# Kernel optimization log

Measured on AMD Instinct MI355X. Metric: run time of the kernel, lower is better.

Reference implementation:

```python
import jax, jax.numpy as jnp
import numpy as np

B, A, NOBS, H1, HX, NACT = 16384, 32, 2, 128, 64, 5
NEIGHBORHOOD = 2.0
GRID_X, GRID_Y = 3, 7


def setup_inputs() -> dict:
    key = jax.random.key(0)
    ks = jax.random.split(key, 6)
    s = 0.1
    return {
        "obs": jax.random.uniform(ks[0], (B, A, NOBS), dtype=jnp.float32),
        # per-agent weights, stored [A, in, out] (torch Linear weight is [out,in])
        "W1": jax.random.normal(ks[1], (A, NOBS, H1), dtype=jnp.float32) * s,
        "b1": jnp.zeros((A, H1), dtype=jnp.float32),
        "W2": jax.random.normal(ks[2], (A, H1, HX), dtype=jnp.float32) * s,
        "b2": jnp.zeros((A, HX), dtype=jnp.float32),
        "Wc": jax.random.normal(ks[3], (A, 2 * HX, HX), dtype=jnp.float32) * s,
        "bc": jnp.zeros((A, HX), dtype=jnp.float32),
        "Wd": jax.random.normal(ks[4], (A, HX, NACT), dtype=jnp.float32) * s,
        "bd": jnp.zeros((A, NACT), dtype=jnp.float32),
    }


def reference(obs, W1, b1, W2, b2, Wc, bc, Wd, bd):
    # --- neighbor mask from L1 distance on rescaled positions ---
    scales = jnp.array([GRID_X - 1.0, GRID_Y - 1.0], dtype=obs.dtype)
    pos = obs * scales  # [B, A, 2]
    dists = jnp.sum(jnp.abs(pos[:, :, None, :] - pos[:, None, :, :]), axis=-1)  # [B, A, A]
    mask = ((dists > 0.0) & (dists < NEIGHBORHOOD)).astype(obs.dtype)  # [B, A, A]

    # --- per-agent encoder MLP: Linear(2,128)+ReLU, Linear(128,64)+ReLU ---
    h = jax.nn.relu(jnp.einsum('bai,aio->bao', obs, W1) + b1)   # [B, A, 128]
    hidden = jax.nn.relu(jnp.einsum('bai,aio->bao', h, W2) + b2)  # [B, A, 64]

    # --- k=1 communication round: masked neighbor mean, then per-agent Linear+Tanh ---
    total = jnp.einsum('baj,bjh->bah', mask, hidden)  # [B, A, 64]
    J = jnp.sum(mask, axis=-1)                         # [B, A]
    J = jnp.where(J > 0.0, J, 1.0)
    comms = total / J[..., None]
    comm_input = jnp.concatenate([hidden, comms], axis=-1)  # [B, A, 128]
    hidden = jnp.tanh(jnp.einsum('bai,aio->bao', comm_input, Wc) + bc)  # [B, A, 64]

    # --- per-agent decoder Linear(64, n_actions) ---
    q = jnp.einsum('bah,aho->bao', hidden, Wd) + bd  # [B, A, NACT]
    return q
```

## Files before the change

### kernel.cpp

```cpp
#include <hip/hip_runtime.h>

#define NAGENTS 32
#define NOBSV   2
#define H1D     128
#define HXD     64
#define NACTD   5

typedef _Float16 h8 __attribute__((ext_vector_type(8)));
typedef float f32x4 __attribute__((ext_vector_type(4)));


__global__ __launch_bounds__(256, 4) void k0_prep(
    const float* __restrict__ W2, const float* __restrict__ Wc,
    h8* __restrict__ wfrag)
{
    const int a = blockIdx.x;
    const int tid = threadIdx.x;
    #pragma unroll
    for (int mat = 0; mat < 2; ++mat) {
        const float* src = (mat == 0 ? W2 : Wc) + (size_t)a * (H1D * HXD);
        h8* dhi = wfrag + ((size_t)(mat * NAGENTS + a) * 2 + 0) * 1024;
        h8* dlo = wfrag + ((size_t)(mat * NAGENTS + a) * 2 + 1) * 1024;
        #pragma unroll
        for (int s4 = 0; s4 < 4; ++s4) {
            const int s  = tid + s4 * 256;
            const int fi = s >> 6, ln = s & 63;
            const int k0  = (fi >> 2) * 32 + (ln >> 4) * 8;
            const int col = (fi & 3) * 16 + (ln & 15);
            h8 whi, wlo;
            #pragma unroll
            for (int j = 0; j < 8; ++j) {
                float w = src[(size_t)(k0 + j) * HXD + col];
                _Float16 hi = (_Float16)w;
                whi[j] = hi;
                wlo[j] = (_Float16)(w - (float)hi);
            }
            dhi[s] = whi;
            dlo[s] = wlo;
        }
    }
}

__global__ __launch_bounds__(256, 4) void k1_encoder(
    const float* __restrict__ obs, const float* __restrict__ W1,
    const float* __restrict__ b1, const float* __restrict__ W2,
    const float* __restrict__ b2, _Float16* __restrict__ ci,
    const h8* __restrict__ wfrag)
{
    __shared__ h8    s_wf[2][16][64];
    __shared__ float s_w1a[H1D], s_w1b[H1D], s_b1[H1D], s_b2[HXD];
    __shared__ float s_ob[128][2];

    const int a   = blockIdx.x;
    const int r0  = blockIdx.y * 128;
    const int tid = threadIdx.x;
    const int wv  = tid >> 6, lane = tid & 63;
    const int l15 = lane & 15, lq = lane >> 4;

    {
        const float* w1p = W1 + a * (NOBSV * H1D);
        if (tid < H1D) {
            s_w1a[tid] = w1p[tid];
            s_w1b[tid] = w1p[H1D + tid];
            s_b1[tid]  = b1[a * H1D + tid];
        } else if (tid < H1D + HXD) {
            s_b2[tid - H1D] = b2[a * HXD + (tid - H1D)];
        }
        if (tid < 128) {
            const float2 ov = *reinterpret_cast<const float2*>(
                obs + ((size_t)(r0 + tid) * NAGENTS + a) * NOBSV);
            s_ob[tid][0] = ov.x; s_ob[tid][1] = ov.y;
        }
        if (wfrag) {
            const h8* srcf = wfrag + (size_t)a * 2048;
            h8* dstf = &s_wf[0][0][0];
            #pragma unroll
            for (int c = 0; c < 8; ++c) dstf[tid + c * 256] = srcf[tid + c * 256];
        } else {
            const float* wsrc = W2 + (size_t)a * (H1D * HXD);
            #pragma unroll
            for (int s4 = 0; s4 < 4; ++s4) {
                const int s  = tid + s4 * 256;
                const int fi = s >> 6, ln = s & 63;
                const int k0  = (fi >> 2) * 32 + (ln >> 4) * 8;
                const int col = (fi & 3) * 16 + (ln & 15);
                h8 whi, wlo;
                #pragma unroll
                for (int j = 0; j < 8; ++j) {
                    float w = wsrc[(size_t)(k0 + j) * HXD + col];
                    _Float16 hi = (_Float16)w;
                    whi[j] = hi;
                    wlo[j] = (_Float16)(w - (float)hi);
                }
                s_wf[0][fi][ln] = whi;
                s_wf[1][fi][ln] = wlo;
            }
        }
    }
    __syncthreads();

    const float o0r0 = s_ob[wv * 32 + l15][0],      o1r0 = s_ob[wv * 32 + l15][1];
    const float o0r1 = s_ob[wv * 32 + 16 + l15][0], o1r1 = s_ob[wv * 32 + 16 + l15][1];

    f32x4 acc[2][4];
    #pragma unroll
    for (int m = 0; m < 2; ++m)
        #pragma unroll
        for (int n = 0; n < 4; ++n) {
            const float bv = s_b2[n * 16 + l15];
            acc[m][n] = (f32x4){bv, bv, bv, bv};
        }
    #pragma unroll
    for (int kt = 0; kt < 4; ++kt) {
        h8 af0, af1;
        #pragma unroll
        for (int j = 0; j < 8; ++j) {
            const int k = kt * 32 + lq * 8 + j;
            const float wa = s_w1a[k], wb = s_w1b[k], bb = s_b1[k];
            af0[j] = (_Float16)fmaxf(fmaf(o1r0, wb, fmaf(o0r0, wa, bb)), 0.0f);
            af1[j] = (_Float16)fmaxf(fmaf(o1r1, wb, fmaf(o0r1, wa, bb)), 0.0f);
        }
        #pragma unroll
        for (int n = 0; n < 4; ++n) {
            h8 bh = s_wf[0][kt * 4 + n][lane];
            h8 bl = s_wf[1][kt * 4 + n][lane];
            acc[0][n] = __builtin_amdgcn_mfma_f32_16x16x32_f16(af0, bh, acc[0][n], 0, 0, 0);
            acc[1][n] = __builtin_amdgcn_mfma_f32_16x16x32_f16(af1, bh, acc[1][n], 0, 0, 0);
            acc[0][n] = __builtin_amdgcn_mfma_f32_16x16x32_f16(af0, bl, acc[0][n], 0, 0, 0);
            acc[1][n] = __builtin_amdgcn_mfma_f32_16x16x32_f16(af1, bl, acc[1][n], 0, 0, 0);
        }
    }
    #pragma unroll
    for (int m = 0; m < 2; ++m)
        #pragma unroll
        for (int r = 0; r < 4; ++r) {
            const int row = wv * 32 + m * 16 + lq * 4 + r;
            _Float16* dst = ci + ((size_t)(r0 + row) * NAGENTS + a) * 128;
            #pragma unroll
            for (int n = 0; n < 4; ++n)
                dst[n * 16 + l15] = (_Float16)fmaxf(acc[m][n][r], 0.0f);
        }
}

__global__ __launch_bounds__(256, 2) void k2_comms(
    const float* __restrict__ obs, _Float16* __restrict__ ci)
{
    __shared__ __align__(16) _Float16 s_tt[8][64][40];
    __shared__ __align__(16) _Float16 s_m[8][32][40];
    __shared__ float s_o[8][66];
    __shared__ float s_J[8][32];

    const int r0  = blockIdx.x * 8;
    const int tid = threadIdx.x;
    const int wv  = tid >> 6, lane = tid & 63;
    const int l15 = lane & 15, lq = lane >> 4;

    if (tid < 128) {
        const float4 v = reinterpret_cast<const float4*>(obs + (size_t)r0 * NAGENTS * NOBSV)[tid];
        const int row = tid >> 4, seg = tid & 15;
        *reinterpret_cast<float4*>(&s_o[row][seg * 4]) = v;
    }
    __syncthreads();

    const int row = tid >> 5;
    const int u   = tid & 31;

    {
        const h8* src = reinterpret_cast<const h8*>(
            ci + ((size_t)(r0 + row) * NAGENTS + u) * 128);
        #pragma unroll
        for (int c = 0; c < 8; ++c) {
            h8 v = src[c];
            #pragma unroll
            for (int e = 0; e < 8; ++e) s_tt[row][c * 8 + e][u] = v[e];
        }
    }
    {
        unsigned int bits = 0u;
        const double xi = (double)s_o[row][u * 2 + 0] * 2.0;
        const double yi = (double)s_o[row][u * 2 + 1] * 6.0;
        #pragma unroll
        for (int j = 0; j < NAGENTS; ++j) {
            double xj = (double)s_o[row][j * 2 + 0] * 2.0;
            double yj = (double)s_o[row][j * 2 + 1] * 6.0;
            double d = fabs(xi - xj) + fabs(yi - yj);
            if (d > 0.0 && d < 2.0) bits |= (1u << j);
        }
        s_J[row][u] = fmaxf((float)__popc(bits), 1.0f);
        #pragma unroll
        for (int c = 0; c < 4; ++c) {
            h8 mv;
            #pragma unroll
            for (int e = 0; e < 8; ++e)
                mv[e] = ((bits >> (c * 8 + e)) & 1u) ? (_Float16)1.0f : (_Float16)0.0f;
            *reinterpret_cast<h8*>(&s_m[row][u][c * 8]) = mv;
        }
    }
    asm volatile("s_waitcnt lgkmcnt(0)" ::: "memory");
    __builtin_amdgcn_sched_barrier(0);

    #pragma unroll
    for (int rr = 0; rr < 2; ++rr) {
        const int rw = wv * 2 + rr;
        h8 a0 = *reinterpret_cast<const h8*>(&s_m[rw][l15][lq * 8]);
        h8 a1 = *reinterpret_cast<const h8*>(&s_m[rw][16 + l15][lq * 8]);
        f32x4 acc[2][4];
        #pragma unroll
        for (int m = 0; m < 2; ++m)
            #pragma unroll
            for (int n = 0; n < 4; ++n) acc[m][n] = (f32x4){0.f, 0.f, 0.f, 0.f};
        #pragma unroll
        for (int n = 0; n < 4; ++n) {
            h8 b = *reinterpret_cast<const h8*>(&s_tt[rw][n * 16 + l15][lq * 8]);
            acc[0][n] = __builtin_amdgcn_mfma_f32_16x16x32_f16(a0, b, acc[0][n], 0, 0, 0);
            acc[1][n] = __builtin_amdgcn_mfma_f32_16x16x32_f16(a1, b, acc[1][n], 0, 0, 0);
        }
        #pragma unroll
        for (int m = 0; m < 2; ++m)
            #pragma unroll
            for (int r = 0; r < 4; ++r) {
                const int ai = m * 16 + lq * 4 + r;
                const float Jv = s_J[rw][ai];
                _Float16* dst = ci + ((size_t)(r0 + rw) * NAGENTS + ai) * 128 + 64;
                #pragma unroll
                for (int n = 0; n < 4; ++n)
                    dst[n * 16 + l15] = (_Float16)(acc[m][n][r] / Jv);
            }
    }
}

__global__ __launch_bounds__(256, 4) void k3_head(
    const _Float16* __restrict__ ci,
    const float* __restrict__ Wc, const float* __restrict__ bc,
    const float* __restrict__ Wd, const float* __restrict__ bd,
    float* __restrict__ out, const h8* __restrict__ wfrag)
{
    __shared__ h8    s_wf[2][16][64];
    __shared__ float s_wd[HXD][8];
    __shared__ float s_bc[HXD];
    __shared__ float s_bd[8];

    const int a   = blockIdx.x;
    const int r0  = blockIdx.y * 128;
    const int tid = threadIdx.x;
    const int wv  = tid >> 6, lane = tid & 63;
    const int l15 = lane & 15, lq = lane >> 4;

    {
        if (wfrag) {
            const h8* srcf = wfrag + (size_t)(NAGENTS + a) * 2048;
            h8* dstf = &s_wf[0][0][0];
            #pragma unroll
            for (int c = 0; c < 8; ++c) dstf[tid + c * 256] = srcf[tid + c * 256];
        } else {
            const float* wsrc = Wc + (size_t)a * (2 * HXD * HXD);
            #pragma unroll
            for (int s4 = 0; s4 < 4; ++s4) {
                const int s  = tid + s4 * 256;
                const int fi = s >> 6, ln = s & 63;
                const int k0  = (fi >> 2) * 32 + (ln >> 4) * 8;
                const int col = (fi & 3) * 16 + (ln & 15);
                h8 whi, wlo;
                #pragma unroll
                for (int j = 0; j < 8; ++j) {
                    float w = wsrc[(size_t)(k0 + j) * HXD + col];
                    _Float16 hi = (_Float16)w;
                    whi[j] = hi;
                    wlo[j] = (_Float16)(w - (float)hi);
                }
                s_wf[0][fi][ln] = whi;
                s_wf[1][fi][ln] = wlo;
            }
        }
        if (tid < HXD) {
            s_bc[tid] = bc[a * HXD + tid];
            #pragma unroll
            for (int o = 0; o < NACTD; ++o)
                s_wd[tid][o] = Wd[(size_t)a * (HXD * NACTD) + tid * NACTD + o];
        } else if (tid < HXD + NACTD) {
            s_bd[tid - HXD] = bd[a * NACTD + (tid - HXD)];
        }
    }
    __syncthreads();

    const _Float16* rb0 = ci + ((size_t)(r0 + wv * 32 + l15) * NAGENTS + a) * 128;
    const _Float16* rb1 = rb0 + (size_t)16 * NAGENTS * 128;

    f32x4 acc[2][4];
    #pragma unroll
    for (int m = 0; m < 2; ++m)
        #pragma unroll
        for (int n = 0; n < 4; ++n) {
            const float bv = s_bc[n * 16 + l15];
            acc[m][n] = (f32x4){bv, bv, bv, bv};
        }
    #pragma unroll
    for (int kt = 0; kt < 4; ++kt) {
        h8 af0 = *reinterpret_cast<const h8*>(rb0 + kt * 32 + lq * 8);
        h8 af1 = *reinterpret_cast<const h8*>(rb1 + kt * 32 + lq * 8);
        #pragma unroll
        for (int n = 0; n < 4; ++n) {
            h8 bh = s_wf[0][kt * 4 + n][lane];
            h8 bl = s_wf[1][kt * 4 + n][lane];
            acc[0][n] = __builtin_amdgcn_mfma_f32_16x16x32_f16(af0, bh, acc[0][n], 0, 0, 0);
            acc[1][n] = __builtin_amdgcn_mfma_f32_16x16x32_f16(af1, bh, acc[1][n], 0, 0, 0);
            acc[0][n] = __builtin_amdgcn_mfma_f32_16x16x32_f16(af0, bl, acc[0][n], 0, 0, 0);
            acc[1][n] = __builtin_amdgcn_mfma_f32_16x16x32_f16(af1, bl, acc[1][n], 0, 0, 0);
        }
    }

    #pragma unroll
    for (int m = 0; m < 2; ++m)
        #pragma unroll
        for (int r = 0; r < 4; ++r) {
            float qv[NACTD];
            #pragma unroll
            for (int o = 0; o < NACTD; ++o) qv[o] = 0.0f;
            #pragma unroll
            for (int n = 0; n < 4; ++n) {
                const float t = tanhf(acc[m][n][r]);
                const float* wd = s_wd[n * 16 + l15];
                #pragma unroll
                for (int o = 0; o < NACTD; ++o) qv[o] = fmaf(t, wd[o], qv[o]);
            }
            #pragma unroll
            for (int o = 0; o < NACTD; ++o) {
                qv[o] += __shfl_xor(qv[o], 1, 64);
                qv[o] += __shfl_xor(qv[o], 2, 64);
                qv[o] += __shfl_xor(qv[o], 4, 64);
                qv[o] += __shfl_xor(qv[o], 8, 64);
            }
            if (l15 == 0) {
                const int row = wv * 32 + m * 16 + lq * 4 + r;
                float* op = out + ((size_t)(r0 + row) * NAGENTS + a) * NACTD;
                #pragma unroll
                for (int o = 0; o < NACTD; ++o) op[o] = qv[o] + s_bd[o];
            }
        }
}

#define TBATCH  8
#define NWAVES  4
#define BFST    2056
#define HROWST  132
__global__ __launch_bounds__(256, 3) void qnet_fused_fb(
    const float* __restrict__ obs,
    const float* __restrict__ W1, const float* __restrict__ b1,
    const float* __restrict__ W2, const float* __restrict__ b2,
    const float* __restrict__ Wc, const float* __restrict__ bc,
    const float* __restrict__ Wd, const float* __restrict__ bd,
    float* __restrict__ out)
{
    __shared__ float    s_obs[TBATCH][NAGENTS * 2 + 2];
    __shared__ _Float16 s_hid[TBATCH * BFST];
    __shared__ float    s_h[NWAVES][TBATCH][HROWST];

    const int tid  = threadIdx.x;
    const int wave = tid >> 6;
    const int lane = tid & 63;
    const int lb   = lane & 7;
    const int og   = lane >> 3;
    const int b0   = blockIdx.x * TBATCH;

    {
        const float2* src = reinterpret_cast<const float2*>(obs + (size_t)b0 * (NAGENTS * NOBSV));
        float2 v = src[tid];
        s_obs[tid >> 5][(tid & 31) * 2 + 0] = v.x;
        s_obs[tid >> 5][(tid & 31) * 2 + 1] = v.y;
    }
    __syncthreads();

    const int p_a = tid >> 3;
    const int p_b = tid & 7;
    unsigned int bits = 0u;
    float Jf;
    {
        const double xi = (double)s_obs[p_b][p_a * 2 + 0] * 2.0;
        const double yi = (double)s_obs[p_b][p_a * 2 + 1] * 6.0;
        #pragma unroll
        for (int j = 0; j < NAGENTS; ++j) {
            double xj = (double)s_obs[p_b][j * 2 + 0] * 2.0;
            double yj = (double)s_obs[p_b][j * 2 + 1] * 6.0;
            double d = fabs(xi - xj) + fabs(yi - yj);
            if (d > 0.0 && d < 2.0) bits |= (1u << j);
        }
        Jf = fmaxf((float)__popc(bits), 1.0f);
    }

    #pragma unroll 1
    for (int ai = 0; ai < 8; ++ai) {
        const int a = wave * 8 + ai;
        const float o0 = s_obs[lb][a * 2 + 0];
        const float o1 = s_obs[lb][a * 2 + 1];
        {
            const float* __restrict__ w1a = W1 + a * (NOBSV * H1D) + og * 16;
            const float* __restrict__ w1b = w1a + H1D;
            const float* __restrict__ b1p = b1 + a * H1D + og * 16;
            float* hdst = &s_h[wave][lb][og * 16];
            #pragma unroll
            for (int c = 0; c < 4; ++c) {
                float4 wa = *reinterpret_cast<const float4*>(w1a + 4 * c);
                float4 wb = *reinterpret_cast<const float4*>(w1b + 4 * c);
                float4 bv = *reinterpret_cast<const float4*>(b1p + 4 * c);
                float4 hv;
                hv.x = fmaxf(fmaf(o1, wb.x, fmaf(o0, wa.x, bv.x)), 0.0f);
                hv.y = fmaxf(fmaf(o1, wb.y, fmaf(o0, wa.y, bv.y)), 0.0f);
                hv.z = fmaxf(fmaf(o1, wb.z, fmaf(o0, wa.z, bv.z)), 0.0f);
                hv.w = fmaxf(fmaf(o1, wb.w, fmaf(o0, wa.w, bv.w)), 0.0f);
                *reinterpret_cast<float4*>(hdst + 4 * c) = hv;
            }
        }
        asm volatile("s_waitcnt lgkmcnt(0)" ::: "memory");
        __builtin_amdgcn_sched_barrier(0);

        const float* __restrict__ w2p = W2 + a * (H1D * HXD) + og * 8;
        const float* __restrict__ b2p = b2 + a * HXD + og * 8;
        float acc[8];
        {
            float4 bv0 = *reinterpret_cast<const float4*>(b2p + 0);
            float4 bv1 = *reinterpret_cast<const float4*>(b2p + 4);
            acc[0] = bv0.x; acc[1] = bv0.y; acc[2] = bv0.z; acc[3] = bv0.w;
            acc[4] = bv1.x; acc[5] = bv1.y; acc[6] = bv1.z; acc[7] = bv1.w;
        }
        const float* hsrc = &s_h[wave][lb][0];
        #pragma unroll 8
        for (int k = 0; k < H1D; ++k) {
            const float hv = hsrc[k];
            const float* wr = w2p + k * HXD;
            float4 wv0 = *reinterpret_cast<const float4*>(wr + 0);
            float4 wv1 = *reinterpret_cast<const float4*>(wr + 4);
            acc[0] = fmaf(hv, wv0.x, acc[0]);
            acc[1] = fmaf(hv, wv0.y, acc[1]);
            acc[2] = fmaf(hv, wv0.z, acc[2]);
            acc[3] = fmaf(hv, wv0.w, acc[3]);
            acc[4] = fmaf(hv, wv1.x, acc[4]);
            acc[5] = fmaf(hv, wv1.y, acc[5]);
            acc[6] = fmaf(hv, wv1.z, acc[6]);
            acc[7] = fmaf(hv, wv1.w, acc[7]);
        }
        h8 hh;
        #pragma unroll
        for (int i = 0; i < 8; ++i) hh[i] = (_Float16)fmaxf(acc[i], 0.0f);
        *reinterpret_cast<h8*>(&s_hid[lb * BFST + a * HXD + og * 8]) = hh;
    }
    __syncthreads();

    #pragma unroll 1
    for (int ai = 0; ai < 8; ++ai) {
        const int a = wave * 8 + ai;
        const int srcm = ai * 8 + lb;
        const unsigned int mbits = (unsigned int)__shfl((int)bits, srcm, 64);
        const float Jv = __shfl(Jf, srcm, 64);

        float cm8[8];
        #pragma unroll
        for (int i = 0; i < 8; ++i) cm8[i] = 0.0f;
        {
            const _Float16* hrow = &s_hid[lb * BFST + og * 8];
            #pragma unroll 8
            for (int j = 0; j < NAGENTS; ++j) {
                const float m = (float)((mbits >> j) & 1u);
                h8 v = *reinterpret_cast<const h8*>(hrow + j * HXD);
                cm8[0] = fmaf(m, (float)v[0], cm8[0]);
                cm8[1] = fmaf(m, (float)v[1], cm8[1]);
                cm8[2] = fmaf(m, (float)v[2], cm8[2]);
                cm8[3] = fmaf(m, (float)v[3], cm8[3]);
                cm8[4] = fmaf(m, (float)v[4], cm8[4]);
                cm8[5] = fmaf(m, (float)v[5], cm8[5]);
                cm8[6] = fmaf(m, (float)v[6], cm8[6]);
                cm8[7] = fmaf(m, (float)v[7], cm8[7]);
            }
        }
        {
            float* cw = &s_h[wave][lb][og * 8];
            *reinterpret_cast<float4*>(cw + 0) =
                make_float4(cm8[0]/Jv, cm8[1]/Jv, cm8[2]/Jv, cm8[3]/Jv);
            *reinterpret_cast<float4*>(cw + 4) =
                make_float4(cm8[4]/Jv, cm8[5]/Jv, cm8[6]/Jv, cm8[7]/Jv);
        }
        asm volatile("s_waitcnt lgkmcnt(0)" ::: "memory");
        __builtin_amdgcn_sched_barrier(0);

        const float* __restrict__ wcp = Wc + a * (2 * HXD * HXD) + og * 8;
        const float* __restrict__ bcp = bc + a * HXD + og * 8;
        float acc[8];
        {
            float4 bv0 = *reinterpret_cast<const float4*>(bcp + 0);
            float4 bv1 = *reinterpret_cast<const float4*>(bcp + 4);
            acc[0] = bv0.x; acc[1] = bv0.y; acc[2] = bv0.z; acc[3] = bv0.w;
            acc[4] = bv1.x; acc[5] = bv1.y; acc[6] = bv1.z; acc[7] = bv1.w;
        }
        const _Float16* hbase = &s_hid[lb * BFST + a * HXD];
        #pragma unroll 8
        for (int k = 0; k < HXD; ++k) {
            const float ci2 = (float)hbase[k];
            const float* wr = wcp + k * HXD;
            float4 wv0 = *reinterpret_cast<const float4*>(wr + 0);
            float4 wv1 = *reinterpret_cast<const float4*>(wr + 4);
            acc[0] = fmaf(ci2, wv0.x, acc[0]);
            acc[1] = fmaf(ci2, wv0.y, acc[1]);
            acc[2] = fmaf(ci2, wv0.z, acc[2]);
            acc[3] = fmaf(ci2, wv0.w, acc[3]);
            acc[4] = fmaf(ci2, wv1.x, acc[4]);
            acc[5] = fmaf(ci2, wv1.y, acc[5]);
            acc[6] = fmaf(ci2, wv1.z, acc[6]);
            acc[7] = fmaf(ci2, wv1.w, acc[7]);
        }
        #pragma unroll 8
        for (int k2 = 0; k2 < HXD; ++k2) {
            const float ci2 = s_h[wave][lb][k2];
            const float* wr = wcp + (HXD + k2) * HXD;
            float4 wv0 = *reinterpret_cast<const float4*>(wr + 0);
            float4 wv1 = *reinterpret_cast<const float4*>(wr + 4);
            acc[0] = fmaf(ci2, wv0.x, acc[0]);
            acc[1] = fmaf(ci2, wv0.y, acc[1]);
            acc[2] = fmaf(ci2, wv0.z, acc[2]);
            acc[3] = fmaf(ci2, wv0.w, acc[3]);
            acc[4] = fmaf(ci2, wv1.x, acc[4]);
            acc[5] = fmaf(ci2, wv1.y, acc[5]);
            acc[6] = fmaf(ci2, wv1.z, acc[6]);
            acc[7] = fmaf(ci2, wv1.w, acc[7]);
        }
        float qv[NACTD];
        #pragma unroll
        for (int o = 0; o < NACTD; ++o) qv[o] = 0.0f;
        const float* __restrict__ wdp = Wd + a * (HXD * NACTD) + og * 8 * NACTD;
        #pragma unroll
        for (int i = 0; i < 8; ++i) {
            float h2 = tanhf(acc[i]);
            #pragma unroll
            for (int o = 0; o < NACTD; ++o)
                qv[o] = fmaf(h2, wdp[i * NACTD + o], qv[o]);
        }
        #pragma unroll
        for (int o = 0; o < NACTD; ++o) {
            qv[o] += __shfl_xor(qv[o], 8, 64);
            qv[o] += __shfl_xor(qv[o], 16, 64);
            qv[o] += __shfl_xor(qv[o], 32, 64);
        }
        if (og == 0) {
            float* op = out + ((size_t)(b0 + lb) * NAGENTS + a) * NACTD;
            const float* bdp = bd + a * NACTD;
            #pragma unroll
            for (int o = 0; o < NACTD; ++o) op[o] = qv[o] + bdp[o];
        }
    }
}

extern "C" void kernel_launch(void* const* d_in, const int* in_sizes, int n_in,
                              void* d_out, int out_size, void* d_ws, size_t ws_size,
                              hipStream_t stream) {
    (void)out_size;
    if (n_in < 9) return;
    const float* obs = (const float*)d_in[0];
    const float* W1  = (const float*)d_in[1];
    const float* b1v = (const float*)d_in[2];
    const float* W2  = (const float*)d_in[3];
    const float* b2v = (const float*)d_in[4];
    const float* Wc  = (const float*)d_in[5];
    const float* bcv = (const float*)d_in[6];
    const float* Wd  = (const float*)d_in[7];
    const float* bdv = (const float*)d_in[8];
    float* out = (float*)d_out;
    const int Btot = in_sizes[0] / (NAGENTS * NOBSV);

    const size_t ciBytes   = (size_t)Btot * NAGENTS * 128 * 2;
    const size_t fragBytes = (size_t)2 * NAGENTS * 2 * 1024 * 16;
    dim3 blk(256);
    if (ws_size >= ciBytes + fragBytes && (Btot % 128) == 0) {
        _Float16* ci = (_Float16*)d_ws;
        h8* wfrag = (h8*)((char*)d_ws + ciBytes);
        k0_prep<<<dim3(NAGENTS), blk, 0, stream>>>(W2, Wc, wfrag);
        k1_encoder<<<dim3(NAGENTS, Btot / 128), blk, 0, stream>>>(
            obs, W1, b1v, W2, b2v, ci, wfrag);
        k2_comms<<<dim3(Btot / 8), blk, 0, stream>>>(obs, ci);
        k3_head<<<dim3(NAGENTS, Btot / 128), blk, 0, stream>>>(
            ci, Wc, bcv, Wd, bdv, out, wfrag);
    } else if (ws_size >= ciBytes && (Btot % 128) == 0) {
        _Float16* ci = (_Float16*)d_ws;
        k1_encoder<<<dim3(NAGENTS, Btot / 128), blk, 0, stream>>>(
            obs, W1, b1v, W2, b2v, ci, (const h8*)nullptr);
        k2_comms<<<dim3(Btot / 8), blk, 0, stream>>>(obs, ci);
        k3_head<<<dim3(NAGENTS, Btot / 128), blk, 0, stream>>>(
            ci, Wc, bcv, Wd, bdv, out, (const h8*)nullptr);
    } else {
        qnet_fused_fb<<<dim3(Btot / TBATCH), dim3(256), 0, stream>>>(
            obs, W1, b1v, W2, b2v, Wc, bcv, Wd, bdv, out);
    }
}
```

Before: 117.5 us.

## Read prepped weight fragments from global memory directly and use fast tanh

The encoder and head kernels no longer stage the 32KB hi/lo fp16 weight fragments in shared memory. Each wave now loads its MFMA B operands straight from the workspace through the cache, and launch bounds rise from 4 to 6 blocks per CU to use the freed LDS for occupancy. The head kernel replaces tanhf with an exp2/rcp approximation, and the comms kernel stores a reciprocal neighbor count so it multiplies instead of divides. The no-prep fallback path is removed. The risks are redundant global/L2 traffic, since every wave re-reads the same fragments, and slightly lower tanh accuracy.

```diff
diff --git a/kernel.cpp b/kernel.cpp
--- a/kernel.cpp
+++ b/kernel.cpp
@@ -9,6 +9,11 @@
 typedef _Float16 h8 __attribute__((ext_vector_type(8)));
 typedef float f32x4 __attribute__((ext_vector_type(4)));
 
+
+static __device__ __forceinline__ float fast_tanh(float x) {
+    float e = __builtin_amdgcn_exp2f(x * 2.885390081777927f);
+    return fmaf(-2.0f, __builtin_amdgcn_rcpf(e + 1.0f), 1.0f);
+}
 
 __global__ __launch_bounds__(256, 4) void k0_prep(
     const float* __restrict__ W2, const float* __restrict__ Wc,
@@ -41,13 +46,11 @@
     }
 }
 
-__global__ __launch_bounds__(256, 4) void k1_encoder(
+__global__ __launch_bounds__(256, 6) void k1_encoder(
     const float* __restrict__ obs, const float* __restrict__ W1,
-    const float* __restrict__ b1, const float* __restrict__ W2,
-    const float* __restrict__ b2, _Float16* __restrict__ ci,
-    const h8* __restrict__ wfrag)
+    const float* __restrict__ b1, const float* __restrict__ b2,
+    _Float16* __restrict__ ci, const h8* __restrict__ wfrag)
 {
-    __shared__ h8    s_wf[2][16][64];
     __shared__ float s_w1a[H1D], s_w1b[H1D], s_b1[H1D], s_b2[HXD];
     __shared__ float s_ob[128][2];
 
@@ -71,33 +74,10 @@
                 obs + ((size_t)(r0 + tid) * NAGENTS + a) * NOBSV);
             s_ob[tid][0] = ov.x; s_ob[tid][1] = ov.y;
         }
-        if (wfrag) {
-            const h8* srcf = wfrag + (size_t)a * 2048;
-            h8* dstf = &s_wf[0][0][0];
-            #pragma unroll
-            for (int c = 0; c < 8; ++c) dstf[tid + c * 256] = srcf[tid + c * 256];
-        } else {
-            const float* wsrc = W2 + (size_t)a * (H1D * HXD);
-            #pragma unroll
-            for (int s4 = 0; s4 < 4; ++s4) {
-                const int s  = tid + s4 * 256;
-                const int fi = s >> 6, ln = s & 63;
-                const int k0  = (fi >> 2) * 32 + (ln >> 4) * 8;
-                const int col = (fi & 3) * 16 + (ln & 15);
-                h8 whi, wlo;
-                #pragma unroll
-                for (int j = 0; j < 8; ++j) {
-                    float w = wsrc[(size_t)(k0 + j) * HXD + col];
-                    _Float16 hi = (_Float16)w;
-                    whi[j] = hi;
-                    wlo[j] = (_Float16)(w - (float)hi);
-                }
-                s_wf[0][fi][ln] = whi;
-                s_wf[1][fi][ln] = wlo;
-            }
-        }
     }
     __syncthreads();
+
+    const h8* wf = wfrag + (size_t)a * 2048;
 
     const float o0r0 = s_ob[wv * 32 + l15][0],      o1r0 = s_ob[wv * 32 + l15][1];
     const float o0r1 = s_ob[wv * 32 + 16 + l15][0], o1r1 = s_ob[wv * 32 + 16 + l15][1];
@@ -122,8 +102,8 @@
         }
         #pragma unroll
         for (int n = 0; n < 4; ++n) {
-            h8 bh = s_wf[0][kt * 4 + n][lane];
-            h8 bl = s_wf[1][kt * 4 + n][lane];
+            h8 bh = wf[(kt * 4 + n) * 64 + lane];
+            h8 bl = wf[1024 + (kt * 4 + n) * 64 + lane];
             acc[0][n] = __builtin_amdgcn_mfma_f32_16x16x32_f16(af0, bh, acc[0][n], 0, 0, 0);
             acc[1][n] = __builtin_amdgcn_mfma_f32_16x16x32_f16(af1, bh, acc[1][n], 0, 0, 0);
             acc[0][n] = __builtin_amdgcn_mfma_f32_16x16x32_f16(af0, bl, acc[0][n], 0, 0, 0);
@@ -148,7 +128,7 @@
     __shared__ __align__(16) _Float16 s_tt[8][64][40];
     __shared__ __align__(16) _Float16 s_m[8][32][40];
     __shared__ float s_o[8][66];
-    __shared__ float s_J[8][32];
+    __shared__ float s_Ji[8][32];
 
     const int r0  = blockIdx.x * 8;
     const int tid = threadIdx.x;
@@ -186,7 +166,7 @@
             double d = fabs(xi - xj) + fabs(yi - yj);
             if (d > 0.0 && d < 2.0) bits |= (1u << j);
         }
-        s_J[row][u] = fmaxf((float)__popc(bits), 1.0f);
+        s_Ji[row][u] = 1.0f / fmaxf((float)__popc(bits), 1.0f);
         #pragma unroll
         for (int c = 0; c < 4; ++c) {
             h8 mv;
@@ -220,22 +200,20 @@
             #pragma unroll
             for (int r = 0; r < 4; ++r) {
                 const int ai = m * 16 + lq * 4 + r;
-                const float Jv = s_J[rw][ai];
+                const float Ji = s_Ji[rw][ai];
                 _Float16* dst = ci + ((size_t)(r0 + rw) * NAGENTS + ai) * 128 + 64;
                 #pragma unroll
                 for (int n = 0; n < 4; ++n)
-                    dst[n * 16 + l15] = (_Float16)(acc[m][n][r] / Jv);
-            }
-    }
-}
-
-__global__ __launch_bounds__(256, 4) void k3_head(
-    const _Float16* __restrict__ ci,
-    const float* __restrict__ Wc, const float* __restrict__ bc,
+                    dst[n * 16 + l15] = (_Float16)(acc[m][n][r] * Ji);
+            }
+    }
+}
+
+__global__ __launch_bounds__(256, 6) void k3_head(
+    const _Float16* __restrict__ ci, const float* __restrict__ bc,
     const float* __restrict__ Wd, const float* __restrict__ bd,
     float* __restrict__ out, const h8* __restrict__ wfrag)
 {
-    __shared__ h8    s_wf[2][16][64];
     __shared__ float s_wd[HXD][8];
     __shared__ float s_bc[HXD];
     __shared__ float s_bd[8];
@@ -247,31 +225,6 @@
     const int l15 = lane & 15, lq = lane >> 4;
 
     {
-        if (wfrag) {
-            const h8* srcf = wfrag + (size_t)(NAGENTS + a) * 2048;
-            h8* dstf = &s_wf[0][0][0];
-            #pragma unroll
-            for (int c = 0; c < 8; ++c) dstf[tid + c * 256] = srcf[tid + c * 256];
-        } else {
-            const float* wsrc = Wc + (size_t)a * (2 * HXD * HXD);
-            #pragma unroll
-            for (int s4 = 0; s4 < 4; ++s4) {
-                const int s  = tid + s4 * 256;
-                const int fi = s >> 6, ln = s & 63;
-                const int k0  = (fi >> 2) * 32 + (ln >> 4) * 8;
-                const int col = (fi & 3) * 16 + (ln & 15);
-                h8 whi, wlo;
-                #pragma unroll
-                for (int j = 0; j < 8; ++j) {
-                    float w = wsrc[(size_t)(k0 + j) * HXD + col];
-                    _Float16 hi = (_Float16)w;
-                    whi[j] = hi;
-                    wlo[j] = (_Float16)(w - (float)hi);
-                }
-                s_wf[0][fi][ln] = whi;
-                s_wf[1][fi][ln] = wlo;
-            }
-        }
         if (tid < HXD) {
             s_bc[tid] = bc[a * HXD + tid];
             #pragma unroll
@@ -283,6 +236,7 @@
     }
     __syncthreads();
 
+    const h8* wf = wfrag + (size_t)(NAGENTS + a) * 2048;
     const _Float16* rb0 = ci + ((size_t)(r0 + wv * 32 + l15) * NAGENTS + a) * 128;
     const _Float16* rb1 = rb0 + (size_t)16 * NAGENTS * 128;
 
@@ -300,8 +254,8 @@
         h8 af1 = *reinterpret_cast<const h8*>(rb1 + kt * 32 + lq * 8);
         #pragma unroll
         for (int n = 0; n < 4; ++n) {
-            h8 bh = s_wf[0][kt * 4 + n][lane];
-            h8 bl = s_wf[1][kt * 4 + n][lane];
+            h8 bh = wf[(kt * 4 + n) * 64 + lane];
+            h8 bl = wf[1024 + (kt * 4 + n) * 64 + lane];
             acc[0][n] = __builtin_amdgcn_mfma_f32_16x16x32_f16(af0, bh, acc[0][n], 0, 0, 0);
             acc[1][n] = __builtin_amdgcn_mfma_f32_16x16x32_f16(af1, bh, acc[1][n], 0, 0, 0);
             acc[0][n] = __builtin_amdgcn_mfma_f32_16x16x32_f16(af0, bl, acc[0][n], 0, 0, 0);
@@ -318,7 +272,7 @@
             for (int o = 0; o < NACTD; ++o) qv[o] = 0.0f;
             #pragma unroll
             for (int n = 0; n < 4; ++n) {
-                const float t = tanhf(acc[m][n][r]);
+                const float t = fast_tanh(acc[m][n][r]);
                 const float* wd = s_wd[n * 16 + l15];
                 #pragma unroll
                 for (int o = 0; o < NACTD; ++o) qv[o] = fmaf(t, wd[o], qv[o]);
@@ -572,17 +526,10 @@
         h8* wfrag = (h8*)((char*)d_ws + ciBytes);
         k0_prep<<<dim3(NAGENTS), blk, 0, stream>>>(W2, Wc, wfrag);
         k1_encoder<<<dim3(NAGENTS, Btot / 128), blk, 0, stream>>>(
-            obs, W1, b1v, W2, b2v, ci, wfrag);
+            obs, W1, b1v, b2v, ci, wfrag);
         k2_comms<<<dim3(Btot / 8), blk, 0, stream>>>(obs, ci);
         k3_head<<<dim3(NAGENTS, Btot / 128), blk, 0, stream>>>(
-            ci, Wc, bcv, Wd, bdv, out, wfrag);
-    } else if (ws_size >= ciBytes && (Btot % 128) == 0) {
-        _Float16* ci = (_Float16*)d_ws;
-        k1_encoder<<<dim3(NAGENTS, Btot / 128), blk, 0, stream>>>(
-            obs, W1, b1v, W2, b2v, ci, (const h8*)nullptr);
-        k2_comms<<<dim3(Btot / 8), blk, 0, stream>>>(obs, ci);
-        k3_head<<<dim3(NAGENTS, Btot / 128), blk, 0, stream>>>(
-            ci, Wc, bcv, Wd, bdv, out, (const h8*)nullptr);
+            ci, bcv, Wd, bdv, out, wfrag);
     } else {
         qnet_fused_fb<<<dim3(Btot / TBATCH), dim3(256), 0, stream>>>(
             obs, W1, b1v, W2, b2v, Wc, bcv, Wd, bdv, out);
```

Measured after the change: 125.8 us. +7.1%, slower.
